# Kernel optimization log

Measured on AMD Instinct MI355X. Metric: run time of the kernel, lower is better.

## Reference

```python
import jax, jax.numpy as jnp
import numpy as np

POOLING_COUNTS = [15, 8, 8]
N_CLIPS = 64


def build_mask_and_indices(pooling_counts, N):
    """Replicates the static index construction in __init__ (pure numpy)."""
    mask2d = np.zeros((N, N), dtype=bool)
    mask2d[np.arange(N), np.arange(N)] = True
    maskij = []
    pool_specs = []  # (kernel, stride) for each level
    for gi, c in enumerate(pooling_counts):
        if gi == 0:
            pool_specs.extend([(2, 1)] * c)
        else:
            pool_specs.extend([(3, 2)] + [(2, 1)] * (c - 1))
    stride, offset = 1, 0
    for c in pooling_counts:
        for _ in range(c):
            offset += stride
            i = np.arange(0, N - offset, stride)
            j = np.arange(offset, N, stride)
            mask2d[i, j] = True
            maskij.append((i, j))
        stride *= 2
    return mask2d, maskij, pool_specs


def maxpool1d(x, k, s):
    # x: [B, D, L]; MaxPool1d(kernel=k, stride=s), no padding
    L = x.shape[-1]
    out_len = (L - k) // s + 1
    idx = np.arange(out_len)[:, None] * s + np.arange(k)[None, :]  # [out_len, k]
    return x[..., idx].max(axis=-1)


def setup_inputs() -> dict:
    key = jax.random.key(0)
    x = jax.random.normal(key, (16, 512, N_CLIPS), dtype=jnp.float32)
    return {"x": x}


def reference(x):
    B, D, N = x.shape
    mask2d_np, maskij, pool_specs = build_mask_and_indices(POOLING_COUNTS, N)
    diag = np.arange(N)

    # diagonal scatter: map2d[:, :, n, n] = x[:, :, n]
    base = jnp.zeros((B, D, N, N), dtype=x.dtype).at[:, :, diag, diag].set(x)

    # boundary map: average of endpoint features at each (i, j) line
    boundary_map2d = base
    for i, j in maskij:
        boundary_map2d = boundary_map2d.at[:, :, i, j].set((x[:, :, i] + x[:, :, j]) * 0.5)

    # content map: pyramid of max-pools scattered onto the same lines
    content_map2d = base
    xp = x
    for (k, s), (i, j) in zip(pool_specs, maskij):
        xp = maxpool1d(xp, k, s)
        content_map2d = content_map2d.at[:, :, i, j].set(xp)

    mask2d = jnp.broadcast_to(jnp.asarray(mask2d_np)[None, None], (B, 1, N, N))
    return boundary_map2d, content_map2d, mask2d
```

## Files before the change

### kernel.cpp

```cpp
#include <hip/hip_runtime.h>


#define T_PER_WAVE 2

__global__ __launch_bounds__(256) void sbc_kernel(const float* __restrict__ x,
                                                  float* __restrict__ out,
                                                  size_t mapsz) {
    const int lane = threadIdx.x & 63;
    const int wid  = blockIdx.x * 4 + (threadIdx.x >> 6);
    const int j    = lane;

    const int sh = 63 - j;
    const unsigned long long mbits =
          (1ULL << j)
        | (0x7FFF000000000000ULL >> sh)
        | ((0x0000555500000000ULL >> sh) & 0x5555555555555555ULL)
        | ((0x0000000011111111ULL >> sh) & 0x1111111111111111ULL);

    const int tile0 = wid * T_PER_WAVE;

    float xv[T_PER_WAVE];
#pragma unroll
    for (int tt = 0; tt < T_PER_WAVE; ++tt)
        xv[tt] = x[(size_t)(tile0 + tt) * 64 + j];

#pragma unroll
    for (int tt = 0; tt < T_PER_WAVE; ++tt) {
        const int tile = tile0 + tt;
        float* __restrict__ bout = out + (size_t)tile * 4096;
        float* __restrict__ cout = bout + mapsz;
        const float xj = xv[tt];
        float r = xj;
#pragma unroll
        for (int i = 63; i >= 0; --i) {
            const float xi = __shfl(xv[tt], i, 64);
            const float xs = (j >= i) ? xi : -INFINITY;
            r = fmaxf(r, xs);
            const bool on  = (mbits >> i) & 1ULL;
            const float s  = on ? 0.5f : 0.0f;
            const float s2 = on ? 1.0f : 0.0f;
            bout[i * 64 + j] = s * (xi + xj);
            cout[i * 64 + j] = s2 * r;
        }
        if ((tile & 511) == 0) {
            float* __restrict__ mout = out + 2 * mapsz + (size_t)(tile >> 9) * 4096;
#pragma unroll
            for (int i = 0; i < 64; ++i)
                mout[i * 64 + j] = ((mbits >> i) & 1ULL) ? 1.0f : 0.0f;
        }
    }
}

extern "C" void kernel_launch(void* const* d_in, const int* in_sizes, int n_in,
                              void* d_out, int out_size, void* d_ws, size_t ws_size,
                              hipStream_t stream) {
    const float* x = (const float*)d_in[0];
    float* out = (float*)d_out;
    const int N  = 64;
    const int BD = in_sizes[0] / N;
    const size_t mapsz = (size_t)BD * N * N;
    const int nwaves = BD / T_PER_WAVE;
    sbc_kernel<<<dim3(nwaves / 4), dim3(256), 0, stream>>>(x, out, mapsz);
}
```

Before: 250.3 us.

## Vectorize map stores to float4 with four tiles per wave

Each lane now handles four adjacent columns, so every boundary and content map row is written with 128-bit float4 stores, and one wave covers four tiles in 16-lane groups. Row values come from a ds_bpermute with component selection, and the running max is reset at each group's diagonal instead of using a -inf mask. The aim is fewer store instructions and wider memory transactions on this write-bound kernel. The cost is more per-lane register state, with each wave doing one pass instead of two tiles.

```diff
diff --git a/kernel.cpp b/kernel.cpp
--- a/kernel.cpp
+++ b/kernel.cpp
@@ -1,52 +1,70 @@
 #include <hip/hip_runtime.h>
 
-
-#define T_PER_WAVE 2
 
 __global__ __launch_bounds__(256) void sbc_kernel(const float* __restrict__ x,
                                                   float* __restrict__ out,
                                                   size_t mapsz) {
     const int lane = threadIdx.x & 63;
     const int wid  = blockIdx.x * 4 + (threadIdx.x >> 6);
-    const int j    = lane;
+    const int g    = lane >> 4;
+    const int cq   = (lane & 15) << 2;
+    const int t0   = wid << 2;
+    const int tile = t0 + g;
 
-    const int sh = 63 - j;
-    const unsigned long long mbits =
-          (1ULL << j)
-        | (0x7FFF000000000000ULL >> sh)
-        | ((0x0000555500000000ULL >> sh) & 0x5555555555555555ULL)
-        | ((0x0000000011111111ULL >> sh) & 0x1111111111111111ULL);
+    unsigned long long mb[4];
+#pragma unroll
+    for (int q = 0; q < 4; ++q) {
+        const int j  = cq + q;
+        const int sh = 63 - j;
+        mb[q] = (1ULL << j)
+              | (0x7FFF000000000000ULL >> sh)
+              | ((0x0000555500000000ULL >> sh) & 0x5555555555555555ULL)
+              | ((0x0000000011111111ULL >> sh) & 0x1111111111111111ULL);
+    }
 
-    const int tile0 = wid * T_PER_WAVE;
+    const float4 xq = *(const float4*)(x + (size_t)tile * 64 + cq);
+    const float xc[4] = {xq.x, xq.y, xq.z, xq.w};
+    float r[4] = {xq.x, xq.y, xq.z, xq.w};
 
-    float xv[T_PER_WAVE];
-#pragma unroll
-    for (int tt = 0; tt < T_PER_WAVE; ++tt)
-        xv[tt] = x[(size_t)(tile0 + tt) * 64 + j];
+    float* __restrict__ bout = out + (size_t)tile * 4096 + cq;
+    float* __restrict__ cout = bout + mapsz;
+
+    const int gbase = (lane & 48) << 2;
 
 #pragma unroll
-    for (int tt = 0; tt < T_PER_WAVE; ++tt) {
-        const int tile = tile0 + tt;
-        float* __restrict__ bout = out + (size_t)tile * 4096;
-        float* __restrict__ cout = bout + mapsz;
-        const float xj = xv[tt];
-        float r = xj;
+    for (int i = 63; i >= 0; --i) {
+        const int src = gbase + (i & ~3);
+        const int comp = i & 3;
+        const float xi = __int_as_float(__builtin_amdgcn_ds_bpermute(
+            src, __float_as_int(comp == 0 ? xq.x : comp == 1 ? xq.y
+                              : comp == 2 ? xq.z : xq.w)));
+
+        float b[4], c[4];
 #pragma unroll
-        for (int i = 63; i >= 0; --i) {
-            const float xi = __shfl(xv[tt], i, 64);
-            const float xs = (j >= i) ? xi : -INFINITY;
-            r = fmaxf(r, xs);
-            const bool on  = (mbits >> i) & 1ULL;
-            const float s  = on ? 0.5f : 0.0f;
-            const float s2 = on ? 1.0f : 0.0f;
-            bout[i * 64 + j] = s * (xi + xj);
-            cout[i * 64 + j] = s2 * r;
+        for (int q = 0; q < 4; ++q) {
+            const float f = fmaxf(r[q], xi);
+            if (q == (i & 3)) {
+                r[q] = (cq == (i & ~3)) ? xc[q] : f;
+            } else {
+                r[q] = f;
+            }
+            const bool on = (mb[q] >> i) & 1ULL;
+            b[q] = on ? 0.5f * (xi + xc[q]) : 0.0f;
+            c[q] = on ? r[q] : 0.0f;
         }
-        if ((tile & 511) == 0) {
-            float* __restrict__ mout = out + 2 * mapsz + (size_t)(tile >> 9) * 4096;
+        *(float4*)(bout + i * 64) = make_float4(b[0], b[1], b[2], b[3]);
+        *(float4*)(cout + i * 64) = make_float4(c[0], c[1], c[2], c[3]);
+    }
+
+    if (((t0 & 511) == 0) && g == 0) {
+        float* __restrict__ mout = out + 2 * mapsz + (size_t)(t0 >> 9) * 4096 + cq;
 #pragma unroll
-            for (int i = 0; i < 64; ++i)
-                mout[i * 64 + j] = ((mbits >> i) & 1ULL) ? 1.0f : 0.0f;
+        for (int i = 0; i < 64; ++i) {
+            float m[4];
+#pragma unroll
+            for (int q = 0; q < 4; ++q)
+                m[q] = ((mb[q] >> i) & 1ULL) ? 1.0f : 0.0f;
+            *(float4*)(mout + i * 64) = make_float4(m[0], m[1], m[2], m[3]);
         }
     }
 }
@@ -59,6 +77,6 @@
     const int N  = 64;
     const int BD = in_sizes[0] / N;
     const size_t mapsz = (size_t)BD * N * N;
-    const int nwaves = BD / T_PER_WAVE;
-    sbc_kernel<<<dim3(nwaves / 4), dim3(256), 0, stream>>>(x, out, mapsz);
+    const int blocks = BD / 16;
+    sbc_kernel<<<dim3(blocks), dim3(256), 0, stream>>>(x, out, mapsz);
 }
```

After: 252.7 us. Within noise of the previous version (+0.9%).
